# Performance work log

Measured on AMD Instinct MI355X. Metric: run time of the kernel, lower is better.

The kernel has to match this reference:

```python
import jax, jax.numpy as jnp
import numpy as np

N = 50000
E = 500000
IN_DIM = 128
HID = 128
EDGE_DIM = 1
MAX_DEPTH = 4  # depth values in [0, MAX_DEPTH]


def setup_inputs() -> dict:
    key = jax.random.key(0)
    ks = jax.random.split(key, 10)
    x = jax.random.normal(ks[0], (N, IN_DIM), jnp.float32)
    edge_index = jax.random.randint(ks[1], (2, E), 0, N)
    edge_attr = jax.random.normal(ks[2], (E, EDGE_DIM), jnp.float32)
    depth = jax.random.randint(ks[3], (N,), 0, MAX_DEPTH + 1)
    def w(k, sh):
        return (jax.random.normal(k, sh, jnp.float32) / np.float32(np.sqrt(sh[0])))
    return {
        "x": x, "edge_index": edge_index, "edge_attr": edge_attr, "depth": depth,
        "pw": w(ks[4], (IN_DIM, HID)), "pb": jnp.zeros((HID,), jnp.float32),
        "mw1": w(ks[5], (HID + EDGE_DIM, HID)), "mb1": jnp.zeros((HID,), jnp.float32),
        "mw2": w(ks[6], (HID, HID)), "mb2": jnp.zeros((HID,), jnp.float32),
        "uw1": w(ks[7], (2 * HID, HID)), "ub1": jnp.zeros((HID,), jnp.float32),
        "uw2": w(ks[8], (HID, HID)), "ub2": jnp.zeros((HID,), jnp.float32),
    }


def reference(x, edge_index, edge_attr, depth, pw, pb, mw1, mb1, mw2, mb2, uw1, ub1, uw2, ub2):
    src, dst = edge_index[0], edge_index[1]
    dst_depth = depth[dst]  # [E]
    h = x @ pw + pb  # node_proj -> [N, HID]
    # Sequential topological DP over depth levels (static unroll, small count).
    for d in range(1, MAX_DEPTH + 1):
        emask = dst_depth == d  # [E]
        # msg_mlp over all edges using current h (lower-depth nodes already updated)
        msg_in = jnp.concatenate([h[src], edge_attr], axis=-1)  # [E, HID+EDGE_DIM]
        msgs = jax.nn.relu(jax.nn.relu(msg_in @ mw1 + mb1) @ mw2 + mb2)
        msgs = jnp.where(emask[:, None], msgs, jnp.zeros((), h.dtype))
        agg = jax.ops.segment_sum(msgs, dst, num_segments=N)  # [N, HID]
        counts = jax.ops.segment_sum(emask.astype(h.dtype), dst, num_segments=N)
        agg = agg / jnp.clip(counts, 1.0)[:, None]  # mean aggregation, clamp(min=1)
        upd_in = jnp.concatenate([h, agg], axis=-1)  # [N, 2*HID]
        h_new = jax.nn.relu(jax.nn.relu(upd_in @ uw1 + ub1) @ uw2 + ub2)
        h = jnp.where((depth == d)[:, None], h_new, h)
    return h
```

## Files before the change

### kernel.cpp

```cpp
#include <hip/hip_runtime.h>

typedef _Float16 f16;
typedef f16 f16x2 __attribute__((ext_vector_type(2)));
typedef f16 f16x8 __attribute__((ext_vector_type(8)));
typedef float f32x4 __attribute__((ext_vector_type(4)));
typedef float f32x2 __attribute__((ext_vector_type(2)));

#define MFMA16(a, b, c) __builtin_amdgcn_mfma_f32_16x16x32_f16((a), (b), (c), 0, 0, 0)

static __device__ __forceinline__ f16x8 cvt8(const float* __restrict__ p) {
    f32x4 p0 = *(const f32x4*)p;
    f32x4 p1 = *(const f32x4*)(p + 4);
    f16x8 a;
    a[0] = (f16)p0[0]; a[1] = (f16)p0[1]; a[2] = (f16)p0[2]; a[3] = (f16)p0[3];
    a[4] = (f16)p1[0]; a[5] = (f16)p1[1]; a[6] = (f16)p1[2]; a[7] = (f16)p1[3];
    return a;
}

__global__ __launch_bounds__(256) void k_prep(
        const float* __restrict__ pw, const float* __restrict__ mw1,
        const float* __restrict__ mw2, const float* __restrict__ uw1,
        const float* __restrict__ uw2,
        f16* __restrict__ pwp, f16* __restrict__ mw1p, f16* __restrict__ mw2p,
        f16* __restrict__ uw1p, f16* __restrict__ uw2p,
        const int* __restrict__ ei, int* __restrict__ degv,
        const int* __restrict__ dep, int* __restrict__ dcnt,
        int4* __restrict__ recs, int CB, int E, int N) {
    __shared__ int lcnt[4];
    __shared__ int lbase[4];
    int b = blockIdx.x;
    int t = threadIdx.x;
    if (b < 48) {
        const float* W; f16* out; int fb;
        if (b < 8)       { W = pw;  out = pwp;  fb = b; }
        else if (b < 16) { W = mw1; out = mw1p; fb = b - 8; }
        else if (b < 24) { W = mw2; out = mw2p; fb = b - 16; }
        else if (b < 40) { W = uw1; out = uw1p; fb = b - 24; }
        else             { W = uw2; out = uw2p; fb = b - 40; }
        int idx = fb * 256 + t;
        int lane = idx & 63;
        int nt = (idx >> 6) & 7;
        int kt = idx >> 9;
        int colx = lane & 15, quad = lane >> 4;
        f16* o = out + (size_t)idx * 8;
        const float* wb = W + (size_t)(kt * 32 + quad * 8) * 128 + nt * 16 + colx;
#pragma unroll
        for (int j = 0; j < 8; j++) o[j] = (f16)wb[(size_t)j * 128];
    } else if (b < 48 + CB) {
        int e = (b - 48) * 256 + t;
        if (e < E) atomicAdd(&degv[ei[E + e]], 1);
    } else {
        if (t < 4) lcnt[t] = 0;
        __syncthreads();
        int v = (b - 48 - CB) * 256 + t;
        int d = (v < N) ? dep[v] : 0;
        int p = -1;
        if (d >= 1 && d <= 4) p = atomicAdd(&lcnt[d - 1], 1);
        __syncthreads();
        if (t < 4) lbase[t] = (lcnt[t] > 0) ? atomicAdd(&dcnt[t], lcnt[t]) : 0;
        __syncthreads();
        if (d >= 1 && d <= 4) recs[(size_t)(d - 1) * N + lbase[d - 1] + p].x = v;
    }
}

__global__ __launch_bounds__(256) void k_mid(
        const int* __restrict__ degv, int* __restrict__ bsum, int SB,
        const float* __restrict__ x, const f16* __restrict__ pwp,
        const f16* __restrict__ mw1p, const float* __restrict__ pb,
        const float* __restrict__ mb1, float* __restrict__ h,
        f16* __restrict__ hh, f16* __restrict__ t, int N) {
    __shared__ __align__(16) f16 lds[4][16 * 136];
    __shared__ int wsum[4];
    int tid = threadIdx.x;
    if ((int)blockIdx.x < SB) {
        int idx = blockIdx.x * 256 + tid;
        int v = (idx < N) ? degv[idx] : 0;
#pragma unroll
        for (int off = 32; off; off >>= 1) v += __shfl_down(v, off, 64);
        if ((tid & 63) == 0) wsum[tid >> 6] = v;
        __syncthreads();
        if (tid == 0) bsum[blockIdx.x] = wsum[0] + wsum[1] + wsum[2] + wsum[3];
        return;
    }
    int lane = tid & 63, w = tid >> 6;
    int colx = lane & 15, quad = lane >> 4;
    int base = ((blockIdx.x - SB) * 4 + w) * 16;
    int arow = base + colx;
    int u = arow < N ? arow : N - 1;

    f32x4 c1[8];
#pragma unroll
    for (int nt = 0; nt < 8; nt++) c1[nt] = (f32x4){0.f, 0.f, 0.f, 0.f};
#pragma unroll
    for (int kt = 0; kt < 4; kt++) {
        f16x8 a = cvt8(x + (size_t)u * 128 + kt * 32 + quad * 8);
#pragma unroll
        for (int nt = 0; nt < 8; nt++) {
            f16x8 b = *(const f16x8*)(pwp + ((size_t)(kt * 8 + nt) * 64 + lane) * 8);
            c1[nt] = MFMA16(a, b, c1[nt]);
        }
    }
#pragma unroll
    for (int nt = 0; nt < 8; nt++) {
        float bias = pb[nt * 16 + colx];
#pragma unroll
        for (int reg = 0; reg < 4; reg++) {
            int row = quad * 4 + reg;
            int node = base + row;
            float v = c1[nt][reg] + bias;
            lds[w][row * 136 + nt * 16 + colx] = (f16)v;
            if (node < N) {
                h[(size_t)node * 128 + nt * 16 + colx] = v;
                hh[(size_t)node * 128 + nt * 16 + colx] = (f16)v;
            }
        }
    }
    f32x4 c2[8];
#pragma unroll
    for (int nt = 0; nt < 8; nt++) c2[nt] = (f32x4){0.f, 0.f, 0.f, 0.f};
#pragma unroll
    for (int kt = 0; kt < 4; kt++) {
        f16x8 a = *(const f16x8*)&lds[w][colx * 136 + kt * 32 + quad * 8];
#pragma unroll
        for (int nt = 0; nt < 8; nt++) {
            f16x8 b = *(const f16x8*)(mw1p + ((size_t)(kt * 8 + nt) * 64 + lane) * 8);
            c2[nt] = MFMA16(a, b, c2[nt]);
        }
    }
#pragma unroll
    for (int nt = 0; nt < 8; nt++) {
        float bias = mb1[nt * 16 + colx];
#pragma unroll
        for (int reg = 0; reg < 4; reg++) {
            int node = base + quad * 4 + reg;
            if (node < N) t[(size_t)node * 128 + nt * 16 + colx] = (f16)(c2[nt][reg] + bias);
        }
    }
}

__global__ __launch_bounds__(256) void k_scanC(const int* __restrict__ degv,
                                               const int* __restrict__ bsum,
                                               int* __restrict__ rowp, int N, int E) {
    __shared__ int lds[256];
    __shared__ int wo[4];
    int b = blockIdx.x, t = threadIdx.x;
    int idx = b * 256 + t;
    int v = (idx < N) ? degv[idx] : 0;
    lds[t] = v;
    __syncthreads();
#pragma unroll
    for (int d = 1; d < 256; d <<= 1) {
        int u = (t >= d) ? lds[t - d] : 0;
        __syncthreads();
        lds[t] += u;
        __syncthreads();
    }
    int off = 0;
    for (int j = t; j < b; j += 256) off += bsum[j];
#pragma unroll
    for (int o = 32; o; o >>= 1) off += __shfl_down(off, o, 64);
    if ((t & 63) == 0) wo[t >> 6] = off;
    __syncthreads();
    int boff = wo[0] + wo[1] + wo[2] + wo[3];
    if (idx < N) rowp[idx] = boff + lds[t] - v;
    if (b == 0 && t == 0) rowp[N] = E;
}

__global__ __launch_bounds__(256) void k_scat(const int* __restrict__ ei,
                                              const float* __restrict__ eattr,
                                              const int* __restrict__ dep,
                                              const int* __restrict__ rowp,
                                              int* __restrict__ cur,
                                              int2* __restrict__ esea,
                                              int4* __restrict__ recs,
                                              const int* __restrict__ dcnt,
                                              int E, int N) {
    int gtid = blockIdx.x * 256 + threadIdx.x;
    int gsz = gridDim.x * 256;
    for (int e = gtid; e < E; e += gsz) {
        int s = ei[e], d = ei[E + e];
        int p = rowp[d] + atomicAdd(&cur[d], 1);
        esea[p] = (int2){s | (dep[s] << 20), __float_as_int(eattr[e])};
    }
    for (int d4 = 0; d4 < 4; d4++) {
        int cnt = dcnt[d4];
        for (int i = gtid; i < cnt; i += gsz) {
            int4* r = &recs[(size_t)d4 * N + i];
            int u = r->x;
            r->y = rowp[u];
            r->z = rowp[u + 1];
        }
    }
}

__global__ __launch_bounds__(512) void k_md(
        const f16* __restrict__ tOrg, f16* __restrict__ tUpd,
        const float* __restrict__ mw1, const float* __restrict__ mb2,
        const f16* __restrict__ mw2p, const int2* __restrict__ esea,
        const int4* __restrict__ recs, const int* __restrict__ dcnt,
        const f16* __restrict__ hh, const f16* __restrict__ uw1p,
        const f16* __restrict__ uw2p, const f16* __restrict__ mw1p,
        const float* __restrict__ ub1, const float* __restrict__ ub2,
        const float* __restrict__ mb1, float* __restrict__ h,
        int dIdx, int N) {
    __shared__ __align__(16) f16 bsm[128 * 128];
    __shared__ __align__(16) f16 tbuf[8][16][136];
    __shared__ __align__(16) f16 pool[16][136];
    __shared__ __align__(16) f16 sout[16][136];
    __shared__ int2 ebuf[8][16];
    __shared__ int ids[16], se0[16], se1[16];
    f16* hbuf = &tbuf[0][0][0];

    const int tid = threadIdx.x;
    const int lane = tid & 63;
    const int w = tid >> 6;
    const int colx = lane & 15, quad = lane >> 4;
    const int cnt = dcnt[dIdx];

    {
        const f16x8* s8 = (const f16x8*)mw2p;
        f16x8* d8 = (f16x8*)bsm;
#pragma unroll
        for (int i = 0; i < 4; i++) d8[i * 512 + tid] = s8[i * 512 + tid];
    }

    const float* w1r = mw1 + 128 * 128;
    f16x8 w1h[4];
#pragma unroll
    for (int kt = 0; kt < 4; kt++) {
        f32x4 q0 = *(const f32x4*)(w1r + kt * 32 + quad * 8);
        f32x4 q1 = *(const f32x4*)(w1r + kt * 32 + quad * 8 + 4);
        w1h[kt][0] = (f16)q0[0]; w1h[kt][1] = (f16)q0[1];
        w1h[kt][2] = (f16)q0[2]; w1h[kt][3] = (f16)q0[3];
        w1h[kt][4] = (f16)q1[0]; w1h[kt][5] = (f16)q1[1];
        w1h[kt][6] = (f16)q1[2]; w1h[kt][7] = (f16)q1[3];
    }
    float mb2v[8];
#pragma unroll
    for (int nt = 0; nt < 8; nt++) mb2v[nt] = mb2[nt * 16 + colx];

    const int b = blockIdx.x, nb = gridDim.x;
    const int s0 = (int)((long long)cnt * b / nb);
    const int s1 = (int)((long long)cnt * (b + 1) / nb);

    auto srow = [&](int sv) -> const f16* {
        const f16* tb = ((unsigned)((sv >> 20) - 1) < (unsigned)dIdx) ? tUpd : tOrg;
        return tb + (size_t)(sv & 0xFFFFF) * 128;
    };

    __syncthreads();

    for (int cs = s0; cs < s1; cs += 16) {
        int cc = s1 - cs; if (cc > 16) cc = 16;
        if (tid < 16) {
            if (tid < cc) {
                int4 r = recs[(size_t)dIdx * N + cs + tid];
                ids[tid] = r.x; se0[tid] = r.y; se1[tid] = r.z;
            } else {
                ids[tid] = 0; se0[tid] = 0; se1[tid] = 0;
            }
        }
        __syncthreads();

        for (int g = 0; g < 2; g++) {
            int maxT = 0;
#pragma unroll
            for (int s = 0; s < 8; s++) {
                int r = g * 8 + s;
                int tc = (se1[r] - se0[r] + 15) >> 4;
                if (tc > maxT) maxT = tc;
            }
            float aggv[8] = {0.f, 0.f, 0.f, 0.f, 0.f, 0.f, 0.f, 0.f};
            for (int rd = 0; rd < maxT; rd++) {
                if (tid < 128) {
                    int s = tid >> 4, j = tid & 15;
                    int r = g * 8 + s;
                    int es = se0[r] + rd * 16 + j;
                    if (es < se1[r]) ebuf[s][j] = esea[es];
                }
                __syncthreads();
#pragma unroll
                for (int it = 0; it < 4; it++) {
                    int task = it * 512 + tid;
                    int row = task >> 4, seg = task & 15;
                    int s = row >> 4, j = row & 15;
                    int r = g * 8 + s;
                    int es = se0[r] + rd * 16 + j;
                    if (es < se1[r]) {
                        int sv = ebuf[s][j].x;
                        *(f16x8*)&tbuf[s][j][seg * 8] =
                            *(const f16x8*)(srow(sv) + seg * 8);
                    }
                }
                __syncthreads();
                {
                    int r = g * 8 + w;
                    int bs = se0[r] + rd * 16;
                    int rem = se1[r] - bs;
                    if (rem > 0) {
                        f16 eah = (f16)__int_as_float(ebuf[w][colx].y);
                        f16x8 afr[4];
#pragma unroll
                        for (int kt = 0; kt < 4; kt++) {
                            f16x8 v = *(const f16x8*)&tbuf[w][colx][kt * 32 + quad * 8];
                            f16x8 o;
#pragma unroll
                            for (int j2 = 0; j2 < 8; j2++) {
                                f16 qv = v[j2] + eah * w1h[kt][j2];
                                o[j2] = qv > (f16)0 ? qv : (f16)0;
                            }
                            afr[kt] = o;
                        }
#pragma unroll
                        for (int nt = 0; nt < 8; nt++) {
                            f32x4 c = (f32x4){0.f, 0.f, 0.f, 0.f};
#pragma unroll
                            for (int kt = 0; kt < 4; kt++) {
                                f16x8 bb = *(const f16x8*)&bsm[((kt * 8 + nt) * 64 + lane) * 8];
                                c = MFMA16(afr[kt], bb, c);
                            }
#pragma unroll
                            for (int reg = 0; reg < 4; reg++)
                                if (quad * 4 + reg < rem)
                                    aggv[nt] += fmaxf(c[reg] + mb2v[nt], 0.f);
                        }
                    }
                }
                __syncthreads();
            }
            {
                int r = g * 8 + w;
                int deg = se1[r] - se0[r];
                float inv = 1.f / (float)(deg > 1 ? deg : 1);
#pragma unroll
                for (int nt = 0; nt < 8; nt++) {
                    float s = aggv[nt];
                    s += __shfl_xor(s, 16, 64);
                    s += __shfl_xor(s, 32, 64);
                    if (quad == 0) pool[r][nt * 16 + colx] = (f16)(s * inv);
                }
            }
        }
        __syncthreads();

        if (tid < 256) {
            int row = tid >> 4, seg = tid & 15;
            *(f16x8*)&hbuf[row * 136 + seg * 8] =
                *(const f16x8*)(hh + (size_t)ids[row] * 128 + seg * 8);
        }
        __syncthreads();

        f32x4 c1 = (f32x4){0.f, 0.f, 0.f, 0.f};
#pragma unroll
        for (int kt = 0; kt < 8; kt++) {
            f16x8 a;
            if (kt < 4)
                a = *(const f16x8*)&hbuf[colx * 136 + kt * 32 + quad * 8];
            else
                a = *(const f16x8*)&pool[colx][(kt - 4) * 32 + quad * 8];
            f16x8 bb = *(const f16x8*)(uw1p + ((size_t)(kt * 8 + w) * 64 + lane) * 8);
            c1 = MFMA16(a, bb, c1);
        }
        {
            float bias = ub1[w * 16 + colx];
#pragma unroll
            for (int reg = 0; reg < 4; reg++) {
                int row = quad * 4 + reg;
                sout[row][w * 16 + colx] = (f16)fmaxf(c1[reg] + bias, 0.f);
            }
        }
        __syncthreads();
        f32x4 c2 = (f32x4){0.f, 0.f, 0.f, 0.f};
#pragma unroll
        for (int kt = 0; kt < 4; kt++) {
            f16x8 a = *(const f16x8*)&sout[colx][kt * 32 + quad * 8];
            f16x8 bb = *(const f16x8*)(uw2p + ((size_t)(kt * 8 + w) * 64 + lane) * 8);
            c2 = MFMA16(a, bb, c2);
        }
        {
            float bias = ub2[w * 16 + colx];
#pragma unroll
            for (int reg = 0; reg < 4; reg++) {
                int row = quad * 4 + reg;
                float v = fmaxf(c2[reg] + bias, 0.f);
                pool[row][w * 16 + colx] = (f16)v;
                if (row < cc)
                    h[(size_t)ids[row] * 128 + w * 16 + colx] = v;
            }
        }
        __syncthreads();
        if (dIdx < 3) {
            f32x4 c3 = (f32x4){0.f, 0.f, 0.f, 0.f};
#pragma unroll
            for (int kt = 0; kt < 4; kt++) {
                f16x8 a = *(const f16x8*)&pool[colx][kt * 32 + quad * 8];
                f16x8 bb = *(const f16x8*)(mw1p + ((size_t)(kt * 8 + w) * 64 + lane) * 8);
                c3 = MFMA16(a, bb, c3);
            }
            float bias = mb1[w * 16 + colx];
#pragma unroll
            for (int reg = 0; reg < 4; reg++) {
                int row = quad * 4 + reg;
                if (row < cc)
                    tUpd[(size_t)ids[row] * 128 + w * 16 + colx] =
                        (f16)(c3[reg] + bias);
            }
        }
        __syncthreads();
    }
}

extern "C" void kernel_launch(void* const* d_in, const int* in_sizes, int n_in,
                              void* d_out, int out_size, void* d_ws, size_t ws_size,
                              hipStream_t stream) {
    const float* x    = (const float*)d_in[0];
    const int*   ei   = (const int*)d_in[1];
    const float* eatt = (const float*)d_in[2];
    const int*   dep  = (const int*)d_in[3];
    const float* pw   = (const float*)d_in[4];
    const float* pb   = (const float*)d_in[5];
    const float* mw1  = (const float*)d_in[6];
    const float* mb1  = (const float*)d_in[7];
    const float* mw2  = (const float*)d_in[8];
    const float* mb2  = (const float*)d_in[9];
    const float* uw1  = (const float*)d_in[10];
    const float* ub1  = (const float*)d_in[11];
    const float* uw2  = (const float*)d_in[12];
    const float* ub2  = (const float*)d_in[13];
    float* h = (float*)d_out;

    int N = in_sizes[3];
    int E = in_sizes[1] / 2;
    int NB = (N + 255) / 256;
    int CB = (E + 255) / 256;

    char* ws = (char*)d_ws;
    size_t o = 0;
    auto alloc = [&](size_t bytes) -> char* {
        char* p = ws + o;
        o += (bytes + 255) & ~(size_t)255;
        return p;
    };
    f16*   t    = (f16*)alloc((size_t)N * 128 * 2);
    f16*   hh   = (f16*)alloc((size_t)N * 128 * 2);
    f16*   tUpd = (f16*)alloc((size_t)N * 128 * 2);
    char*  z0   = (char*)alloc(0);
    int*   degv = (int*)alloc((size_t)N * 4);
    int*   cur  = (int*)alloc((size_t)N * 4);
    int*   dcnt = (int*)alloc(64);
    size_t zbytes = (size_t)((char*)alloc(0) - z0);
    int*   rowp = (int*)alloc((size_t)(N + 1) * 4);
    int*   bsum = (int*)alloc((size_t)NB * 4);
    int2*  esea = (int2*)alloc((size_t)E * 8);
    int4*  recs = (int4*)alloc((size_t)4 * N * 16);
    f16*   pwp  = (f16*)alloc(128 * 128 * 2);
    f16*   mw1p = (f16*)alloc(128 * 128 * 2);
    f16*   mw2p = (f16*)alloc(128 * 128 * 2);
    f16*   uw1p = (f16*)alloc(256 * 128 * 2);
    f16*   uw2p = (f16*)alloc(128 * 128 * 2);

    hipMemsetAsync(z0, 0, zbytes, stream);

    k_prep<<<48 + CB + NB, 256, 0, stream>>>(pw, mw1, mw2, uw1, uw2,
                                             pwp, mw1p, mw2p, uw1p, uw2p,
                                             ei, degv, dep, dcnt, recs, CB, E, N);
    int PB = (N + 63) / 64;
    k_mid<<<NB + PB, 256, 0, stream>>>(degv, bsum, NB, x, pwp, mw1p, pb, mb1,
                                       h, hh, t, N);
    k_scanC<<<NB, 256, 0, stream>>>(degv, bsum, rowp, N, E);
    k_scat<<<CB, 256, 0, stream>>>(ei, eatt, dep, rowp, cur, esea, recs, dcnt, E, N);

    for (int d = 0; d < 4; d++) {
        k_md<<<512, 512, 0, stream>>>(t, tUpd, mw1, mb2, mw2p, esea, recs, dcnt,
                                      hh, uw1p, uw2p, mw1p, ub1, ub2, mb1, h,
                                      d, N);
    }
}
```

Measured before the change: 345.7 us.

## Fuse all stages into one persistent kernel with grid-wide barriers

```diff
diff --git a/kernel.cpp b/kernel.cpp
--- a/kernel.cpp
+++ b/kernel.cpp
@@ -7,6 +7,9 @@
 typedef float f32x2 __attribute__((ext_vector_type(2)));
 
 #define MFMA16(a, b, c) __builtin_amdgcn_mfma_f32_16x16x32_f16((a), (b), (c), 0, 0, 0)
+
+#define NBLK 256
+#define NTHR 512
 
 static __device__ __forceinline__ f16x8 cvt8(const float* __restrict__ p) {
     f32x4 p0 = *(const f32x4*)p;
@@ -17,205 +20,209 @@
     return a;
 }
 
-__global__ __launch_bounds__(256) void k_prep(
-        const float* __restrict__ pw, const float* __restrict__ mw1,
-        const float* __restrict__ mw2, const float* __restrict__ uw1,
-        const float* __restrict__ uw2,
-        f16* __restrict__ pwp, f16* __restrict__ mw1p, f16* __restrict__ mw2p,
-        f16* __restrict__ uw1p, f16* __restrict__ uw2p,
-        const int* __restrict__ ei, int* __restrict__ degv,
-        const int* __restrict__ dep, int* __restrict__ dcnt,
-        int4* __restrict__ recs, int CB, int E, int N) {
-    __shared__ int lcnt[4];
-    __shared__ int lbase[4];
-    int b = blockIdx.x;
-    int t = threadIdx.x;
-    if (b < 48) {
-        const float* W; f16* out; int fb;
-        if (b < 8)       { W = pw;  out = pwp;  fb = b; }
-        else if (b < 16) { W = mw1; out = mw1p; fb = b - 8; }
-        else if (b < 24) { W = mw2; out = mw2p; fb = b - 16; }
-        else if (b < 40) { W = uw1; out = uw1p; fb = b - 24; }
-        else             { W = uw2; out = uw2p; fb = b - 40; }
-        int idx = fb * 256 + t;
-        int lane = idx & 63;
-        int nt = (idx >> 6) & 7;
-        int kt = idx >> 9;
-        int colx = lane & 15, quad = lane >> 4;
-        f16* o = out + (size_t)idx * 8;
-        const float* wb = W + (size_t)(kt * 32 + quad * 8) * 128 + nt * 16 + colx;
-#pragma unroll
-        for (int j = 0; j < 8; j++) o[j] = (f16)wb[(size_t)j * 128];
-    } else if (b < 48 + CB) {
-        int e = (b - 48) * 256 + t;
-        if (e < E) atomicAdd(&degv[ei[E + e]], 1);
-    } else {
-        if (t < 4) lcnt[t] = 0;
-        __syncthreads();
-        int v = (b - 48 - CB) * 256 + t;
-        int d = (v < N) ? dep[v] : 0;
-        int p = -1;
-        if (d >= 1 && d <= 4) p = atomicAdd(&lcnt[d - 1], 1);
-        __syncthreads();
-        if (t < 4) lbase[t] = (lcnt[t] > 0) ? atomicAdd(&dcnt[t], lcnt[t]) : 0;
-        __syncthreads();
-        if (d >= 1 && d <= 4) recs[(size_t)(d - 1) * N + lbase[d - 1] + p].x = v;
-    }
+static __device__ __forceinline__ void gsync(unsigned* gb, int k) {
+    __syncthreads();
+    if (threadIdx.x == 0) {
+        unsigned* cnt = gb + k * 64;
+        unsigned* flag = gb + k * 64 + 32;
+        unsigned gen = __hip_atomic_load(flag, __ATOMIC_RELAXED, __HIP_MEMORY_SCOPE_AGENT);
+        unsigned old = __hip_atomic_fetch_add(cnt, 1u, __ATOMIC_ACQ_REL, __HIP_MEMORY_SCOPE_AGENT);
+        if (old == NBLK - 1u) {
+            __hip_atomic_store(cnt, 0u, __ATOMIC_RELAXED, __HIP_MEMORY_SCOPE_AGENT);
+            __hip_atomic_fetch_add(flag, 1u, __ATOMIC_RELEASE, __HIP_MEMORY_SCOPE_AGENT);
+        } else {
+            while (__hip_atomic_load(flag, __ATOMIC_ACQUIRE, __HIP_MEMORY_SCOPE_AGENT) == gen)
+                __builtin_amdgcn_s_sleep(2);
+        }
+    }
+    __syncthreads();
 }
 
-__global__ __launch_bounds__(256) void k_mid(
-        const int* __restrict__ degv, int* __restrict__ bsum, int SB,
-        const float* __restrict__ x, const f16* __restrict__ pwp,
-        const f16* __restrict__ mw1p, const float* __restrict__ pb,
-        const float* __restrict__ mb1, float* __restrict__ h,
-        f16* __restrict__ hh, f16* __restrict__ t, int N) {
-    __shared__ __align__(16) f16 lds[4][16 * 136];
-    __shared__ int wsum[4];
-    int tid = threadIdx.x;
-    if ((int)blockIdx.x < SB) {
-        int idx = blockIdx.x * 256 + tid;
-        int v = (idx < N) ? degv[idx] : 0;
-#pragma unroll
-        for (int off = 32; off; off >>= 1) v += __shfl_down(v, off, 64);
-        if ((tid & 63) == 0) wsum[tid >> 6] = v;
-        __syncthreads();
-        if (tid == 0) bsum[blockIdx.x] = wsum[0] + wsum[1] + wsum[2] + wsum[3];
-        return;
-    }
-    int lane = tid & 63, w = tid >> 6;
-    int colx = lane & 15, quad = lane >> 4;
-    int base = ((blockIdx.x - SB) * 4 + w) * 16;
-    int arow = base + colx;
-    int u = arow < N ? arow : N - 1;
-
-    f32x4 c1[8];
-#pragma unroll
-    for (int nt = 0; nt < 8; nt++) c1[nt] = (f32x4){0.f, 0.f, 0.f, 0.f};
-#pragma unroll
-    for (int kt = 0; kt < 4; kt++) {
-        f16x8 a = cvt8(x + (size_t)u * 128 + kt * 32 + quad * 8);
-#pragma unroll
-        for (int nt = 0; nt < 8; nt++) {
-            f16x8 b = *(const f16x8*)(pwp + ((size_t)(kt * 8 + nt) * 64 + lane) * 8);
-            c1[nt] = MFMA16(a, b, c1[nt]);
-        }
-    }
-#pragma unroll
-    for (int nt = 0; nt < 8; nt++) {
-        float bias = pb[nt * 16 + colx];
-#pragma unroll
-        for (int reg = 0; reg < 4; reg++) {
-            int row = quad * 4 + reg;
-            int node = base + row;
-            float v = c1[nt][reg] + bias;
-            lds[w][row * 136 + nt * 16 + colx] = (f16)v;
-            if (node < N) {
-                h[(size_t)node * 128 + nt * 16 + colx] = v;
-                hh[(size_t)node * 128 + nt * 16 + colx] = (f16)v;
-            }
-        }
-    }
-    f32x4 c2[8];
-#pragma unroll
-    for (int nt = 0; nt < 8; nt++) c2[nt] = (f32x4){0.f, 0.f, 0.f, 0.f};
-#pragma unroll
-    for (int kt = 0; kt < 4; kt++) {
-        f16x8 a = *(const f16x8*)&lds[w][colx * 136 + kt * 32 + quad * 8];
-#pragma unroll
-        for (int nt = 0; nt < 8; nt++) {
-            f16x8 b = *(const f16x8*)(mw1p + ((size_t)(kt * 8 + nt) * 64 + lane) * 8);
-            c2[nt] = MFMA16(a, b, c2[nt]);
-        }
-    }
-#pragma unroll
-    for (int nt = 0; nt < 8; nt++) {
-        float bias = mb1[nt * 16 + colx];
-#pragma unroll
-        for (int reg = 0; reg < 4; reg++) {
-            int node = base + quad * 4 + reg;
-            if (node < N) t[(size_t)node * 128 + nt * 16 + colx] = (f16)(c2[nt][reg] + bias);
-        }
-    }
-}
-
-__global__ __launch_bounds__(256) void k_scanC(const int* __restrict__ degv,
-                                               const int* __restrict__ bsum,
-                                               int* __restrict__ rowp, int N, int E) {
-    __shared__ int lds[256];
-    __shared__ int wo[4];
-    int b = blockIdx.x, t = threadIdx.x;
-    int idx = b * 256 + t;
-    int v = (idx < N) ? degv[idx] : 0;
-    lds[t] = v;
-    __syncthreads();
-#pragma unroll
-    for (int d = 1; d < 256; d <<= 1) {
-        int u = (t >= d) ? lds[t - d] : 0;
-        __syncthreads();
-        lds[t] += u;
-        __syncthreads();
-    }
-    int off = 0;
-    for (int j = t; j < b; j += 256) off += bsum[j];
-#pragma unroll
-    for (int o = 32; o; o >>= 1) off += __shfl_down(off, o, 64);
-    if ((t & 63) == 0) wo[t >> 6] = off;
-    __syncthreads();
-    int boff = wo[0] + wo[1] + wo[2] + wo[3];
-    if (idx < N) rowp[idx] = boff + lds[t] - v;
-    if (b == 0 && t == 0) rowp[N] = E;
-}
-
-__global__ __launch_bounds__(256) void k_scat(const int* __restrict__ ei,
-                                              const float* __restrict__ eattr,
-                                              const int* __restrict__ dep,
-                                              const int* __restrict__ rowp,
-                                              int* __restrict__ cur,
-                                              int2* __restrict__ esea,
-                                              int4* __restrict__ recs,
-                                              const int* __restrict__ dcnt,
-                                              int E, int N) {
-    int gtid = blockIdx.x * 256 + threadIdx.x;
-    int gsz = gridDim.x * 256;
-    for (int e = gtid; e < E; e += gsz) {
-        int s = ei[e], d = ei[E + e];
-        int p = rowp[d] + atomicAdd(&cur[d], 1);
-        esea[p] = (int2){s | (dep[s] << 20), __float_as_int(eattr[e])};
-    }
-    for (int d4 = 0; d4 < 4; d4++) {
-        int cnt = dcnt[d4];
-        for (int i = gtid; i < cnt; i += gsz) {
-            int4* r = &recs[(size_t)d4 * N + i];
-            int u = r->x;
-            r->y = rowp[u];
-            r->z = rowp[u + 1];
-        }
-    }
-}
-
-__global__ __launch_bounds__(512) void k_md(
-        const f16* __restrict__ tOrg, f16* __restrict__ tUpd,
-        const float* __restrict__ mw1, const float* __restrict__ mb2,
-        const f16* __restrict__ mw2p, const int2* __restrict__ esea,
-        const int4* __restrict__ recs, const int* __restrict__ dcnt,
-        const f16* __restrict__ hh, const f16* __restrict__ uw1p,
-        const f16* __restrict__ uw2p, const f16* __restrict__ mw1p,
-        const float* __restrict__ ub1, const float* __restrict__ ub2,
-        const float* __restrict__ mb1, float* __restrict__ h,
-        int dIdx, int N) {
+__global__ __launch_bounds__(512) void k_all(
+        const float* __restrict__ x, const int* __restrict__ ei,
+        const float* __restrict__ eattr, const int* __restrict__ dep,
+        const float* __restrict__ pw, const float* __restrict__ pb,
+        const float* __restrict__ mw1, const float* __restrict__ mb1,
+        const float* __restrict__ mw2, const float* __restrict__ mb2,
+        const float* __restrict__ uw1, const float* __restrict__ ub1,
+        const float* __restrict__ uw2, const float* __restrict__ ub2,
+        float* __restrict__ h, f16* __restrict__ tOrg, f16* __restrict__ hh,
+        f16* __restrict__ tUpd, unsigned* gb, int* degv, int* cur, int* dcnt,
+        int* rowp, int* bsum, int2* esea, int4* recs,
+        f16* pwp, f16* mw1p, f16* mw2p, f16* uw1p, f16* uw2p,
+        int N, int E) {
     __shared__ __align__(16) f16 bsm[128 * 128];
     __shared__ __align__(16) f16 tbuf[8][16][136];
     __shared__ __align__(16) f16 pool[16][136];
     __shared__ __align__(16) f16 sout[16][136];
     __shared__ int2 ebuf[8][16];
     __shared__ int ids[16], se0[16], se1[16];
-    f16* hbuf = &tbuf[0][0][0];
+    __shared__ int sarr[512];
+    __shared__ int lcnt[4], lbase[4];
 
     const int tid = threadIdx.x;
     const int lane = tid & 63;
     const int w = tid >> 6;
     const int colx = lane & 15, quad = lane >> 4;
-    const int cnt = dcnt[dIdx];
+    const int b = blockIdx.x;
+    const int gtid = b * NTHR + tid;
+    const int gsz = NBLK * NTHR;
+
+    if (b < 24) {
+        int item = b * 512 + tid;
+        int wb = item >> 8;
+        int t8 = item & 255;
+        const float* W; f16* out; int fb;
+        if (wb < 8)       { W = pw;  out = pwp;  fb = wb; }
+        else if (wb < 16) { W = mw1; out = mw1p; fb = wb - 8; }
+        else if (wb < 24) { W = mw2; out = mw2p; fb = wb - 16; }
+        else if (wb < 40) { W = uw1; out = uw1p; fb = wb - 24; }
+        else              { W = uw2; out = uw2p; fb = wb - 40; }
+        int idx = fb * 256 + t8;
+        int lane2 = idx & 63;
+        int nt = (idx >> 6) & 7;
+        int kt = idx >> 9;
+        int cx = lane2 & 15, qd = lane2 >> 4;
+        f16* o = out + (size_t)idx * 8;
+        const float* wbp = W + (size_t)(kt * 32 + qd * 8) * 128 + nt * 16 + cx;
+#pragma unroll
+        for (int j = 0; j < 8; j++) o[j] = (f16)wbp[(size_t)j * 128];
+    } else {
+        int NCB = (N + 511) >> 9;
+        int cb = b - 24;
+        if (cb < NCB) {
+            if (tid < 4) lcnt[tid] = 0;
+            __syncthreads();
+            int v = cb * 512 + tid;
+            int d = (v < N) ? dep[v] : 0;
+            int p = -1;
+            if (d >= 1 && d <= 4) p = atomicAdd(&lcnt[d - 1], 1);
+            __syncthreads();
+            if (tid < 4) lbase[tid] = (lcnt[tid] > 0) ? atomicAdd(&dcnt[tid], lcnt[tid]) : 0;
+            __syncthreads();
+            if (d >= 1 && d <= 4) recs[(size_t)(d - 1) * N + lbase[d - 1] + p].x = v;
+        }
+    }
+    for (int e = gtid; e < E; e += gsz) atomicAdd(&degv[ei[E + e]], 1);
+    gsync(gb, 0);
+
+    const int SEG = (N + NBLK - 1) / NBLK;
+    {
+        int i = b * SEG + tid;
+        int v = (tid < SEG && i < N) ? degv[i] : 0;
+        sarr[tid] = v;
+        __syncthreads();
+#pragma unroll
+        for (int s = 256; s > 0; s >>= 1) {
+            if (tid < s) sarr[tid] += sarr[tid + s];
+            __syncthreads();
+        }
+        if (tid == 0) bsum[b] = sarr[0];
+    }
+    gsync(gb, 1);
+
+    {
+        int bsumb = bsum[b];
+        sarr[tid] = (tid < NBLK) ? bsum[tid] : 0;
+        __syncthreads();
+#pragma unroll
+        for (int d = 1; d < 512; d <<= 1) {
+            int u = (tid >= d) ? sarr[tid - d] : 0;
+            __syncthreads();
+            sarr[tid] += u;
+            __syncthreads();
+        }
+        int base = sarr[b] - bsumb;
+        __syncthreads();
+        int i = b * SEG + tid;
+        int v = (tid < SEG && i < N) ? degv[i] : 0;
+        sarr[tid] = v;
+        __syncthreads();
+#pragma unroll
+        for (int d = 1; d < 512; d <<= 1) {
+            int u = (tid >= d) ? sarr[tid - d] : 0;
+            __syncthreads();
+            sarr[tid] += u;
+            __syncthreads();
+        }
+        if (tid < SEG && i < N) rowp[i] = base + sarr[tid] - v;
+        if (b == 0 && tid == 0) rowp[N] = E;
+    }
+    gsync(gb, 2);
+
+    for (int e = gtid; e < E; e += gsz) {
+        int s = ei[e], dn = ei[E + e];
+        int p = rowp[dn] + atomicAdd(&cur[dn], 1);
+        esea[p] = (int2){s | (dep[s] << 20), __float_as_int(eattr[e])};
+    }
+    for (int d4 = 0; d4 < 4; d4++) {
+        int cntd = dcnt[d4];
+        for (int i = gtid; i < cntd; i += gsz) {
+            int4* r = &recs[(size_t)d4 * N + i];
+            int u = r->x;
+            r->y = rowp[u];
+            r->z = rowp[u + 1];
+        }
+    }
+    {
+        f16* plds = &tbuf[w][0][0];
+        int ntile = (N + 15) >> 4;
+        for (int tile = b * 8 + w; tile < ntile; tile += NBLK * 8) {
+            int base = tile * 16;
+            int arow = base + colx;
+            int u = arow < N ? arow : N - 1;
+            f32x4 c1[8];
+#pragma unroll
+            for (int nt = 0; nt < 8; nt++) c1[nt] = (f32x4){0.f, 0.f, 0.f, 0.f};
+#pragma unroll
+            for (int kt = 0; kt < 4; kt++) {
+                f16x8 a = cvt8(x + (size_t)u * 128 + kt * 32 + quad * 8);
+#pragma unroll
+                for (int nt = 0; nt < 8; nt++) {
+                    f16x8 bb = *(const f16x8*)(pwp + ((size_t)(kt * 8 + nt) * 64 + lane) * 8);
+                    c1[nt] = MFMA16(a, bb, c1[nt]);
+                }
+            }
+#pragma unroll
+            for (int nt = 0; nt < 8; nt++) {
+                float bias = pb[nt * 16 + colx];
+#pragma unroll
+                for (int reg = 0; reg < 4; reg++) {
+                    int row = quad * 4 + reg;
+                    int node = base + row;
+                    float v = c1[nt][reg] + bias;
+                    plds[row * 136 + nt * 16 + colx] = (f16)v;
+                    if (node < N) {
+                        h[(size_t)node * 128 + nt * 16 + colx] = v;
+                        hh[(size_t)node * 128 + nt * 16 + colx] = (f16)v;
+                    }
+                }
+            }
+            f32x4 c2[8];
+#pragma unroll
+            for (int nt = 0; nt < 8; nt++) c2[nt] = (f32x4){0.f, 0.f, 0.f, 0.f};
+#pragma unroll
+            for (int kt = 0; kt < 4; kt++) {
+                f16x8 a = *(const f16x8*)&plds[colx * 136 + kt * 32 + quad * 8];
+#pragma unroll
+                for (int nt = 0; nt < 8; nt++) {
+                    f16x8 bb = *(const f16x8*)(mw1p + ((size_t)(kt * 8 + nt) * 64 + lane) * 8);
+                    c2[nt] = MFMA16(a, bb, c2[nt]);
+                }
+            }
+#pragma unroll
+            for (int nt = 0; nt < 8; nt++) {
+                float bias = mb1[nt * 16 + colx];
+#pragma unroll
+                for (int reg = 0; reg < 4; reg++) {
+                    int node = base + quad * 4 + reg;
+                    if (node < N)
+                        tOrg[(size_t)node * 128 + nt * 16 + colx] = (f16)(c2[nt][reg] + bias);
+                }
+            }
+        }
+    }
+    gsync(gb, 3);
 
     {
         const f16x8* s8 = (const f16x8*)mw2p;
@@ -223,7 +230,6 @@
 #pragma unroll
         for (int i = 0; i < 4; i++) d8[i * 512 + tid] = s8[i * 512 + tid];
     }
-
     const float* w1r = mw1 + 128 * 128;
     f16x8 w1h[4];
 #pragma unroll
@@ -238,175 +244,177 @@
     float mb2v[8];
 #pragma unroll
     for (int nt = 0; nt < 8; nt++) mb2v[nt] = mb2[nt * 16 + colx];
-
-    const int b = blockIdx.x, nb = gridDim.x;
-    const int s0 = (int)((long long)cnt * b / nb);
-    const int s1 = (int)((long long)cnt * (b + 1) / nb);
-
-    auto srow = [&](int sv) -> const f16* {
-        const f16* tb = ((unsigned)((sv >> 20) - 1) < (unsigned)dIdx) ? tUpd : tOrg;
-        return tb + (size_t)(sv & 0xFFFFF) * 128;
-    };
-
+    f16* hbuf = &tbuf[0][0][0];
     __syncthreads();
 
-    for (int cs = s0; cs < s1; cs += 16) {
-        int cc = s1 - cs; if (cc > 16) cc = 16;
-        if (tid < 16) {
-            if (tid < cc) {
-                int4 r = recs[(size_t)dIdx * N + cs + tid];
-                ids[tid] = r.x; se0[tid] = r.y; se1[tid] = r.z;
-            } else {
-                ids[tid] = 0; se0[tid] = 0; se1[tid] = 0;
-            }
-        }
-        __syncthreads();
-
-        for (int g = 0; g < 2; g++) {
-            int maxT = 0;
-#pragma unroll
-            for (int s = 0; s < 8; s++) {
-                int r = g * 8 + s;
-                int tc = (se1[r] - se0[r] + 15) >> 4;
-                if (tc > maxT) maxT = tc;
-            }
-            float aggv[8] = {0.f, 0.f, 0.f, 0.f, 0.f, 0.f, 0.f, 0.f};
-            for (int rd = 0; rd < maxT; rd++) {
-                if (tid < 128) {
-                    int s = tid >> 4, j = tid & 15;
+    for (int dI = 0; dI < 4; dI++) {
+        const int cnt = dcnt[dI];
+        const int s0 = (int)((long long)cnt * b / NBLK);
+        const int s1 = (int)((long long)cnt * (b + 1) / NBLK);
+        auto srow = [&](int sv) -> const f16* {
+            const f16* tb = ((unsigned)((sv >> 20) - 1) < (unsigned)dI) ? tUpd : tOrg;
+            return tb + (size_t)(sv & 0xFFFFF) * 128;
+        };
+
+        for (int cs = s0; cs < s1; cs += 16) {
+            int cc = s1 - cs; if (cc > 16) cc = 16;
+            if (tid < 16) {
+                if (tid < cc) {
+                    int4 r = recs[(size_t)dI * N + cs + tid];
+                    ids[tid] = r.x; se0[tid] = r.y; se1[tid] = r.z;
+                } else {
+                    ids[tid] = 0; se0[tid] = 0; se1[tid] = 0;
+                }
+            }
+            __syncthreads();
+
+            for (int g = 0; g < 2; g++) {
+                int maxT = 0;
+#pragma unroll
+                for (int s = 0; s < 8; s++) {
                     int r = g * 8 + s;
-                    int es = se0[r] + rd * 16 + j;
-                    if (es < se1[r]) ebuf[s][j] = esea[es];
-                }
-                __syncthreads();
-#pragma unroll
-                for (int it = 0; it < 4; it++) {
-                    int task = it * 512 + tid;
-                    int row = task >> 4, seg = task & 15;
-                    int s = row >> 4, j = row & 15;
-                    int r = g * 8 + s;
-                    int es = se0[r] + rd * 16 + j;
-                    if (es < se1[r]) {
-                        int sv = ebuf[s][j].x;
-                        *(f16x8*)&tbuf[s][j][seg * 8] =
-                            *(const f16x8*)(srow(sv) + seg * 8);
+                    int tc = (se1[r] - se0[r] + 15) >> 4;
+                    if (tc > maxT) maxT = tc;
+                }
+                float aggv[8] = {0.f, 0.f, 0.f, 0.f, 0.f, 0.f, 0.f, 0.f};
+                for (int rd = 0; rd < maxT; rd++) {
+                    if (tid < 128) {
+                        int s = tid >> 4, j = tid & 15;
+                        int r = g * 8 + s;
+                        int es = se0[r] + rd * 16 + j;
+                        if (es < se1[r]) ebuf[s][j] = esea[es];
                     }
-                }
-                __syncthreads();
+                    __syncthreads();
+#pragma unroll
+                    for (int it = 0; it < 4; it++) {
+                        int task = it * 512 + tid;
+                        int row = task >> 4, seg = task & 15;
+                        int s = row >> 4, j = row & 15;
+                        int r = g * 8 + s;
+                        int es = se0[r] + rd * 16 + j;
+                        if (es < se1[r]) {
+                            int sv = ebuf[s][j].x;
+                            *(f16x8*)&tbuf[s][j][seg * 8] =
+                                *(const f16x8*)(srow(sv) + seg * 8);
+                        }
+                    }
+                    __syncthreads();
+                    {
+                        int r = g * 8 + w;
+                        int bs = se0[r] + rd * 16;
+                        int rem = se1[r] - bs;
+                        if (rem > 0) {
+                            f16 eah = (f16)__int_as_float(ebuf[w][colx].y);
+                            f16x8 afr[4];
+#pragma unroll
+                            for (int kt = 0; kt < 4; kt++) {
+                                f16x8 v = *(const f16x8*)&tbuf[w][colx][kt * 32 + quad * 8];
+                                f16x8 o;
+#pragma unroll
+                                for (int j2 = 0; j2 < 8; j2++) {
+                                    f16 qv = v[j2] + eah * w1h[kt][j2];
+                                    o[j2] = qv > (f16)0 ? qv : (f16)0;
+                                }
+                                afr[kt] = o;
+                            }
+#pragma unroll
+                            for (int nt = 0; nt < 8; nt++) {
+                                f32x4 c = (f32x4){0.f, 0.f, 0.f, 0.f};
+#pragma unroll
+                                for (int kt = 0; kt < 4; kt++) {
+                                    f16x8 bb = *(const f16x8*)&bsm[((kt * 8 + nt) * 64 + lane) * 8];
+                                    c = MFMA16(afr[kt], bb, c);
+                                }
+#pragma unroll
+                                for (int reg = 0; reg < 4; reg++)
+                                    if (quad * 4 + reg < rem)
+                                        aggv[nt] += fmaxf(c[reg] + mb2v[nt], 0.f);
+                            }
+                        }
+                    }
+                    __syncthreads();
+                }
                 {
                     int r = g * 8 + w;
-                    int bs = se0[r] + rd * 16;
-                    int rem = se1[r] - bs;
-                    if (rem > 0) {
-                        f16 eah = (f16)__int_as_float(ebuf[w][colx].y);
-                        f16x8 afr[4];
-#pragma unroll
-                        for (int kt = 0; kt < 4; kt++) {
-                            f16x8 v = *(const f16x8*)&tbuf[w][colx][kt * 32 + quad * 8];
-                            f16x8 o;
-#pragma unroll
-                            for (int j2 = 0; j2 < 8; j2++) {
-                                f16 qv = v[j2] + eah * w1h[kt][j2];
-                                o[j2] = qv > (f16)0 ? qv : (f16)0;
-                            }
-                            afr[kt] = o;
-                        }
-#pragma unroll
-                        for (int nt = 0; nt < 8; nt++) {
-                            f32x4 c = (f32x4){0.f, 0.f, 0.f, 0.f};
-#pragma unroll
-                            for (int kt = 0; kt < 4; kt++) {
-                                f16x8 bb = *(const f16x8*)&bsm[((kt * 8 + nt) * 64 + lane) * 8];
-                                c = MFMA16(afr[kt], bb, c);
-                            }
-#pragma unroll
-                            for (int reg = 0; reg < 4; reg++)
-                                if (quad * 4 + reg < rem)
-                                    aggv[nt] += fmaxf(c[reg] + mb2v[nt], 0.f);
-                        }
+                    int deg = se1[r] - se0[r];
+                    float inv = 1.f / (float)(deg > 1 ? deg : 1);
+#pragma unroll
+                    for (int nt = 0; nt < 8; nt++) {
+                        float s = aggv[nt];
+                        s += __shfl_xor(s, 16, 64);
+                        s += __shfl_xor(s, 32, 64);
+                        if (quad == 0) pool[r][nt * 16 + colx] = (f16)(s * inv);
                     }
                 }
-                __syncthreads();
+            }
+            __syncthreads();
+
+            if (tid < 256) {
+                int row = tid >> 4, seg = tid & 15;
+                *(f16x8*)&hbuf[row * 136 + seg * 8] =
+                    *(const f16x8*)(hh + (size_t)ids[row] * 128 + seg * 8);
+            }
+            __syncthreads();
+
+            f32x4 c1 = (f32x4){0.f, 0.f, 0.f, 0.f};
+#pragma unroll
+            for (int kt = 0; kt < 8; kt++) {
+                f16x8 a;
+                if (kt < 4)
+                    a = *(const f16x8*)&hbuf[colx * 136 + kt * 32 + quad * 8];
+                else
+                    a = *(const f16x8*)&pool[colx][(kt - 4) * 32 + quad * 8];
+                f16x8 bb = *(const f16x8*)(uw1p + ((size_t)(kt * 8 + w) * 64 + lane) * 8);
+                c1 = MFMA16(a, bb, c1);
             }
             {
-                int r = g * 8 + w;
-                int deg = se1[r] - se0[r];
-                float inv = 1.f / (float)(deg > 1 ? deg : 1);
-#pragma unroll
-                for (int nt = 0; nt < 8; nt++) {
-                    float s = aggv[nt];
-                    s += __shfl_xor(s, 16, 64);
-                    s += __shfl_xor(s, 32, 64);
-                    if (quad == 0) pool[r][nt * 16 + colx] = (f16)(s * inv);
-                }
-            }
-        }
-        __syncthreads();
-
-        if (tid < 256) {
-            int row = tid >> 4, seg = tid & 15;
-            *(f16x8*)&hbuf[row * 136 + seg * 8] =
-                *(const f16x8*)(hh + (size_t)ids[row] * 128 + seg * 8);
-        }
-        __syncthreads();
-
-        f32x4 c1 = (f32x4){0.f, 0.f, 0.f, 0.f};
-#pragma unroll
-        for (int kt = 0; kt < 8; kt++) {
-            f16x8 a;
-            if (kt < 4)
-                a = *(const f16x8*)&hbuf[colx * 136 + kt * 32 + quad * 8];
-            else
-                a = *(const f16x8*)&pool[colx][(kt - 4) * 32 + quad * 8];
-            f16x8 bb = *(const f16x8*)(uw1p + ((size_t)(kt * 8 + w) * 64 + lane) * 8);
-            c1 = MFMA16(a, bb, c1);
-        }
-        {
-            float bias = ub1[w * 16 + colx];
-#pragma unroll
-            for (int reg = 0; reg < 4; reg++) {
-                int row = quad * 4 + reg;
-                sout[row][w * 16 + colx] = (f16)fmaxf(c1[reg] + bias, 0.f);
-            }
-        }
-        __syncthreads();
-        f32x4 c2 = (f32x4){0.f, 0.f, 0.f, 0.f};
-#pragma unroll
-        for (int kt = 0; kt < 4; kt++) {
-            f16x8 a = *(const f16x8*)&sout[colx][kt * 32 + quad * 8];
-            f16x8 bb = *(const f16x8*)(uw2p + ((size_t)(kt * 8 + w) * 64 + lane) * 8);
-            c2 = MFMA16(a, bb, c2);
-        }
-        {
-            float bias = ub2[w * 16 + colx];
-#pragma unroll
-            for (int reg = 0; reg < 4; reg++) {
-                int row = quad * 4 + reg;
-                float v = fmaxf(c2[reg] + bias, 0.f);
-                pool[row][w * 16 + colx] = (f16)v;
-                if (row < cc)
-                    h[(size_t)ids[row] * 128 + w * 16 + colx] = v;
-            }
-        }
-        __syncthreads();
-        if (dIdx < 3) {
-            f32x4 c3 = (f32x4){0.f, 0.f, 0.f, 0.f};
+                float bias = ub1[w * 16 + colx];
+#pragma unroll
+                for (int reg = 0; reg < 4; reg++) {
+                    int row = quad * 4 + reg;
+                    sout[row][w * 16 + colx] = (f16)fmaxf(c1[reg] + bias, 0.f);
+                }
+            }
+            __syncthreads();
+            f32x4 c2 = (f32x4){0.f, 0.f, 0.f, 0.f};
 #pragma unroll
             for (int kt = 0; kt < 4; kt++) {
-                f16x8 a = *(const f16x8*)&pool[colx][kt * 32 + quad * 8];
-                f16x8 bb = *(const f16x8*)(mw1p + ((size_t)(kt * 8 + w) * 64 + lane) * 8);
-                c3 = MFMA16(a, bb, c3);
-            }
-            float bias = mb1[w * 16 + colx];
-#pragma unroll
-            for (int reg = 0; reg < 4; reg++) {
-                int row = quad * 4 + reg;
-                if (row < cc)
-                    tUpd[(size_t)ids[row] * 128 + w * 16 + colx] =
-                        (f16)(c3[reg] + bias);
-            }
-        }
-        __syncthreads();
+                f16x8 a = *(const f16x8*)&sout[colx][kt * 32 + quad * 8];
+                f16x8 bb = *(const f16x8*)(uw2p + ((size_t)(kt * 8 + w) * 64 + lane) * 8);
+                c2 = MFMA16(a, bb, c2);
+            }
+            {
+                float bias = ub2[w * 16 + colx];
+#pragma unroll
+                for (int reg = 0; reg < 4; reg++) {
+                    int row = quad * 4 + reg;
+                    float v = fmaxf(c2[reg] + bias, 0.f);
+                    pool[row][w * 16 + colx] = (f16)v;
+                    if (row < cc)
+                        h[(size_t)ids[row] * 128 + w * 16 + colx] = v;
+                }
+            }
+            __syncthreads();
+            if (dI < 3) {
+                f32x4 c3 = (f32x4){0.f, 0.f, 0.f, 0.f};
+#pragma unroll
+                for (int kt = 0; kt < 4; kt++) {
+                    f16x8 a = *(const f16x8*)&pool[colx][kt * 32 + quad * 8];
+                    f16x8 bb = *(const f16x8*)(mw1p + ((size_t)(kt * 8 + w) * 64 + lane) * 8);
+                    c3 = MFMA16(a, bb, c3);
+                }
+                float bias = mb1[w * 16 + colx];
+#pragma unroll
+                for (int reg = 0; reg < 4; reg++) {
+                    int row = quad * 4 + reg;
+                    if (row < cc)
+                        tUpd[(size_t)ids[row] * 128 + w * 16 + colx] =
+                            (f16)(c3[reg] + bias);
+                }
+            }
+            __syncthreads();
+        }
+        if (dI < 3) gsync(gb, 4 + dI);
     }
 }
 
@@ -431,8 +439,6 @@
 
     int N = in_sizes[3];
     int E = in_sizes[1] / 2;
-    int NB = (N + 255) / 256;
-    int CB = (E + 255) / 256;
 
     char* ws = (char*)d_ws;
     size_t o = 0;
@@ -445,12 +451,13 @@
     f16*   hh   = (f16*)alloc((size_t)N * 128 * 2);
     f16*   tUpd = (f16*)alloc((size_t)N * 128 * 2);
     char*  z0   = (char*)alloc(0);
+    unsigned* gbarr = (unsigned*)alloc(8 * 64 * 4);
     int*   degv = (int*)alloc((size_t)N * 4);
     int*   cur  = (int*)alloc((size_t)N * 4);
     int*   dcnt = (int*)alloc(64);
     size_t zbytes = (size_t)((char*)alloc(0) - z0);
     int*   rowp = (int*)alloc((size_t)(N + 1) * 4);
-    int*   bsum = (int*)alloc((size_t)NB * 4);
+    int*   bsum = (int*)alloc((size_t)NBLK * 4);
     int2*  esea = (int2*)alloc((size_t)E * 8);
     int4*  recs = (int4*)alloc((size_t)4 * N * 16);
     f16*   pwp  = (f16*)alloc(128 * 128 * 2);
@@ -461,18 +468,9 @@
 
     hipMemsetAsync(z0, 0, zbytes, stream);
 
-    k_prep<<<48 + CB + NB, 256, 0, stream>>>(pw, mw1, mw2, uw1, uw2,
-                                             pwp, mw1p, mw2p, uw1p, uw2p,
-                                             ei, degv, dep, dcnt, recs, CB, E, N);
-    int PB = (N + 63) / 64;
-    k_mid<<<NB + PB, 256, 0, stream>>>(degv, bsum, NB, x, pwp, mw1p, pb, mb1,
-                                       h, hh, t, N);
-    k_scanC<<<NB, 256, 0, stream>>>(degv, bsum, rowp, N, E);
-    k_scat<<<CB, 256, 0, stream>>>(ei, eatt, dep, rowp, cur, esea, recs, dcnt, E, N);
-
-    for (int d = 0; d < 4; d++) {
-        k_md<<<512, 512, 0, stream>>>(t, tUpd, mw1, mb2, mw2p, esea, recs, dcnt,
-                                      hh, uw1p, uw2p, mw1p, ub1, ub2, mb1, h,
-                                      d, N);
-    }
+    k_all<<<NBLK, NTHR, 0, stream>>>(x, ei, eatt, dep, pw, pb, mw1, mb1,
+                                     mw2, mb2, uw1, ub1, uw2, ub2,
+                                     h, t, hh, tUpd, gbarr, degv, cur, dcnt,
+                                     rowp, bsum, esea, recs,
+                                     pwp, mw1p, mw2p, uw1p, uw2p, N, E);
 }
```

Result: slower. 542.7 us (+57.0%).
